# Performance work log

Hardware: AMD Instinct MI355X
Metric: run time of the kernel (lower is better)

## Reference

```python
import jax, jax.numpy as jnp
import numpy as np
from jax import lax

B, C, H, W = 2, 256, 64, 64
KC, RD = C // 8, C // 16  # key_channels=32, GatherExcite rd_channels=16
EPS = 1e-5


def setup_inputs() -> dict:
    key = jax.random.key(0)
    ks = jax.random.split(key, 17)
    s = 0.05
    n = lambda k, shp: jax.random.normal(k, shp, jnp.float32) * s
    return {
        "x": jax.random.normal(ks[0], (B, C, H, W), jnp.float32),
        "Wq": n(ks[1], (KC, C)),
        "Wk": n(ks[2], (KC, C)),
        "Wv": n(ks[3], (C, C)),
        "Wb1": n(ks[4], (KC, C)),
        "Wb2": n(ks[5], (KC, C)),
        "w_gb": jax.random.normal(ks[6], (), jnp.float32),  # 1x1 conv on 1-channel bias map
        "ge_w1": n(ks[7], (RD, C)),
        "ge_b1": jnp.zeros((RD,), jnp.float32),
        "ge_w2": n(ks[8], (C, RD)),
        "ge_b2": jnp.zeros((C,), jnp.float32),
        "Wo": n(ks[9], (C, C)),
        "bn_scale": jnp.ones((C,), jnp.float32),
        "bn_bias": jnp.zeros((C,), jnp.float32),
        "bn_mean": jax.random.normal(ks[10], (C,), jnp.float32) * 0.01,
        "bn_var": jnp.ones((C,), jnp.float32),
        "gamma": jax.random.normal(ks[11], (), jnp.float32) * 0.1,
    }


def _conv1x1(t, w):  # t: [B,Cin,H,W], w: [Cout,Cin]
    return jnp.einsum('bchw,oc->bohw', t, w)


def reference(x, Wq, Wk, Wv, Wb1, Wb2, w_gb, ge_w1, ge_b1, ge_w2, ge_b2,
              Wo, bn_scale, bn_bias, bn_mean, bn_var, gamma):
    b, c, h, w = x.shape
    hw = h * w

    # GatherExcite (extent=0, use_mlp=True, gate=sigmoid): global mean -> ConvMlp -> sigmoid gate
    m = x.mean(axis=(2, 3), keepdims=True)                     # [B,C,1,1]
    g = jax.nn.relu(_conv1x1(m, ge_w1) + ge_b1[None, :, None, None])
    g = _conv1x1(g, ge_w2) + ge_b2[None, :, None, None]
    key_in = x * jax.nn.sigmoid(g)                             # [B,C,H,W]

    value = _conv1x1(x, Wv).reshape(b, c, hw).transpose(0, 2, 1)   # [B,HW,C]
    query = _conv1x1(x, Wq).reshape(b, KC, hw).transpose(0, 2, 1)  # [B,HW,Kc]
    key_f = _conv1x1(key_in, Wk).reshape(b, KC, hw)                # [B,Kc,HW]

    sim = jnp.einsum('bnk,bkm->bnm', query, key_f)                 # [B,HW,HW]

    # bias branch (dropout is identity at eval)
    b1 = jax.nn.relu(_conv1x1(x, Wb1)).reshape(b, KC, hw)          # [B,Kc,HW]
    b2 = jax.nn.relu(_conv1x1(x, Wb2)).reshape(b, KC, hw)          # [B,Kc,HW]
    bias = jnp.einsum('bkn,bkm->bnm', b1, b2)                      # [B,HW,HW]

    # AvgPool2d(k=3, s=1, pad=1, count_include_pad=True) on [B,1,HW,HW]
    pooled = lax.reduce_window(bias[:, None], 0.0, lax.add,
                               (1, 1, 3, 3), (1, 1, 1, 1),
                               [(0, 0), (0, 0), (1, 1), (1, 1)]) / 9.0
    bias_map = jax.nn.sigmoid(w_gb * pooled)[:, 0]                 # [B,HW,HW]

    attn = jax.nn.softmax(sim * bias_map, axis=-1)                 # [B,HW,HW]
    ctx = jnp.einsum('bnm,bmc->bnc', attn, value)                  # [B,HW,C]
    ctx = ctx.transpose(0, 2, 1).reshape(b, c, h, w)

    # W: conv1x1 -> BatchNorm (inference) -> ReLU
    y = _conv1x1(ctx, Wo)
    y = (y - bn_mean[None, :, None, None]) * (bn_scale / jnp.sqrt(bn_var + EPS))[None, :, None, None] \
        + bn_bias[None, :, None, None]
    y = jax.nn.relu(y)

    return gamma * y + x
```

## Files before the change

kernel.cpp:

```cpp
#include <hip/hip_runtime.h>
#include <hip/hip_bf16.h>

typedef __bf16 bf16;
typedef __bf16 v8bf __attribute__((ext_vector_type(8)));
typedef __bf16 v4bf __attribute__((ext_vector_type(4)));
typedef float v4f __attribute__((ext_vector_type(4)));

#define HW 4096
#define CH 256
#define KC 32
#define RD 16
#define NB 2
#define BNEPS 1e-5f
#define VSTRIDE 4224
#define LOG2E 1.4426950408889634f

__device__ __forceinline__ float fexp2(float x) {
#if __has_builtin(__builtin_amdgcn_exp2f)
  return __builtin_amdgcn_exp2f(x);
#else
  return exp2f(x);
#endif
}
__device__ __forceinline__ float frcp(float x) {
#if __has_builtin(__builtin_amdgcn_rcpf)
  return __builtin_amdgcn_rcpf(x);
#else
  return 1.f / x;
#endif
}

#define OFF_MEAN   0u
#define OFF_WKB    4096u
#define OFF_QT     69632u
#define OFF_KT     593920u
#define OFF_BS1    1118208u
#define OFF_BS2    1642496u
#define OFF_VT     2166784u
#define OFF_B1R    6492160u
#define OFF_B2R    7016448u
#define OFF_CTX    7540736u
#define OFF_PACC   11735040u
#define OFF_PL     45289472u
#define OFF_WOBF   45551616u
#define OFF_XBT    45682688u
#define OFF_WALL   49876992u

__global__ __launch_bounds__(256) void k_mean(const float* __restrict__ x,
                                              float* __restrict__ mean) {
  int bc = blockIdx.x;
  const float* px = x + (size_t)bc * HW;
  float s = 0.f;
  for (int i = threadIdx.x; i < HW; i += 256) s += px[i];
  __shared__ float red[256];
  red[threadIdx.x] = s; __syncthreads();
  for (int st = 128; st > 0; st >>= 1) {
    if (threadIdx.x < st) red[threadIdx.x] += red[threadIdx.x + st];
    __syncthreads();
  }
  if (threadIdx.x == 0) mean[bc] = red[0] * (1.0f / HW);
}

__global__ __launch_bounds__(256) void k_gate(const float* __restrict__ mean,
    const float* __restrict__ gw1, const float* __restrict__ gb1,
    const float* __restrict__ gw2, const float* __restrict__ gb2,
    const float* __restrict__ Wk, float* __restrict__ wkb,
    const float* __restrict__ Wo, bf16* __restrict__ wo_bf) {
  if (blockIdx.x >= 2) {
    int i = (blockIdx.x - 2) * 256 + threadIdx.x;
    wo_bf[i] = (bf16)Wo[i];
    return;
  }
  int b = blockIdx.x;
  int t = threadIdx.x;
  __shared__ float ms[CH];
  __shared__ float hid[RD];
  ms[t] = mean[b * CH + t];
  __syncthreads();
  if (t < RD) {
    float a = gb1[t];
    for (int c = 0; c < CH; ++c) a += gw1[t * CH + c] * ms[c];
    hid[t] = fmaxf(a, 0.f);
  }
  __syncthreads();
  float a = gb2[t];
  #pragma unroll
  for (int r = 0; r < RD; ++r) a += gw2[t * RD + r] * hid[r];
  float s = 1.f / (1.f + __expf(-a));
  for (int kk = 0; kk < KC; ++kk)
    wkb[((size_t)b * KC + kk) * CH + t] = Wk[kk * CH + t] * s;
}

__global__ __launch_bounds__(256) void k_prep(const float* __restrict__ x,
    const float* __restrict__ Wq, const float* __restrict__ wkb,
    const float* __restrict__ Wb1, const float* __restrict__ Wb2,
    const float* __restrict__ Wv,
    bf16* __restrict__ xbt, bf16* __restrict__ wall) {
  __shared__ __align__(16) float ts[64][68];
  const int blk = blockIdx.x;
  const int t = threadIdx.x;
  if (blk < 512) {
    const int b  = blk >> 8;
    const int id = blk & 255;
    const int ct = id >> 6, nt = id & 63;
    const int c0 = ct * 64, n0 = nt * 64;
    const int crow = t >> 2, nch = (t & 3) * 16;
    const float* xp = x + ((size_t)(b * CH + c0 + crow)) * HW + n0 + nch;
    #pragma unroll
    for (int i = 0; i < 4; ++i)
      *(v4f*)&ts[crow][nch + i * 4] = *(const v4f*)(xp + i * 4);
    __syncthreads();
    const int nl = t >> 2, cc0 = (t & 3) * 16;
    bf16* dst = xbt + ((size_t)(b * HW + n0 + nl)) * CH + c0 + cc0;
    v8bf o0, o1;
    #pragma unroll
    for (int j = 0; j < 8; ++j) { o0[j] = (bf16)ts[cc0 + j][nl]; o1[j] = (bf16)ts[cc0 + 8 + j][nl]; }
    *(v8bf*)dst = o0;
    *(v8bf*)(dst + 8) = o1;
  } else {
    const int idx = blk - 512;
    const int b = idx / 384, row = idx % 384;
    float v;
    if (row < 32)       v = Wq[row * CH + t] * LOG2E;
    else if (row < 64)  v = wkb[((size_t)b * KC + row - 32) * CH + t];
    else if (row < 96)  v = Wb1[(row - 64) * CH + t];
    else if (row < 128) v = Wb2[(row - 96) * CH + t];
    else                v = Wv[(row - 128) * CH + t];
    wall[((size_t)b * 384 + row) * CH + t] = (bf16)v;
  }
}

__global__ __launch_bounds__(256, 4) void k_proj(
    const bf16* __restrict__ xbt, const bf16* __restrict__ wall,
    bf16* __restrict__ qt, bf16* __restrict__ kt,
    bf16* __restrict__ b1r, bf16* __restrict__ b2r, bf16* __restrict__ vt) {
  __shared__ __align__(16) bf16 xs[32][264];
  __shared__ __align__(16) bf16 tr[4][16][24];
  const int blk = blockIdx.x;
  const int b  = blk >> 9;
  const int bm = (blk >> 7) & 3;
  const int nt = blk & 127;
  const int n0 = nt * 32;
  const int t = threadIdx.x;
  {
    const int row = t >> 3, c0 = (t & 7) * 32;
    const bf16* src = xbt + ((size_t)(b * HW + n0 + row)) * CH + c0;
    #pragma unroll
    for (int i = 0; i < 4; ++i)
      *(v8bf*)&xs[row][c0 + i * 8] = *(const v8bf*)(src + i * 8);
  }
  __syncthreads();
  const int w = t >> 6, lane = t & 63, cl = lane & 15, kh = lane >> 4;
  const int nsub = (w & 1) * 16;
  const int otrio = (w >> 1) * 3;
  const v4f vzero = {0.f, 0.f, 0.f, 0.f};
  v4f acc[3] = {vzero, vzero, vzero};
  const bf16* wb = wall + ((size_t)b * 384 + bm * 96) * CH;
  for (int kk = 0; kk < 8; ++kk) {
    v8bf bx = *(const v8bf*)&xs[nsub + cl][kk * 32 + kh * 8];
    #pragma unroll
    for (int j = 0; j < 3; ++j) {
      v8bf af = *(const v8bf*)(wb + (size_t)((otrio + j) * 16 + cl) * CH + kk * 32 + kh * 8);
      acc[j] = __builtin_amdgcn_mfma_f32_16x16x32_bf16(af, bx, acc[j], 0, 0, 0);
    }
  }
  const int n = n0 + nsub + cl;
  #pragma unroll
  for (int j = 0; j < 3; ++j) {
    const int o0 = bm * 96 + (otrio + j) * 16;
    if (o0 < 128) {
      const bool rel = (o0 >= 64);
      v4bf pk;
      #pragma unroll
      for (int r = 0; r < 4; ++r) {
        float v = acc[j][r];
        if (rel) v = fmaxf(v, 0.f);
        pk[r] = (bf16)v;
      }
      const int seg = o0 >> 5;
      bf16* base = seg == 0 ? qt : seg == 1 ? kt : seg == 2 ? b1r : b2r;
      *(v4bf*)&base[((size_t)b * HW + n) * KC + (o0 & 31) + kh * 4] = pk;
    } else {
      #pragma unroll
      for (int r = 0; r < 4; ++r) tr[w][kh * 4 + r][cl] = (bf16)acc[j][r];
      asm volatile("s_waitcnt lgkmcnt(0)" ::: "memory");
      __builtin_amdgcn_sched_barrier(0);
      const int row = lane >> 2, nch = (lane & 3) * 4;
      v4bf d = *(const v4bf*)&tr[w][row][nch];
      *(v4bf*)&vt[((size_t)b * CH + (o0 - 128) + row) * VSTRIDE + n0 + nsub + nch] = d;
    }
  }
}

__global__ __launch_bounds__(256) void k_pool(const bf16* __restrict__ b1r,
    const bf16* __restrict__ b2r, const float* __restrict__ wgb,
    bf16* __restrict__ bs1, bf16* __restrict__ bs2) {
  int i = blockIdx.x * 256 + threadIdx.x;
  int n = (i >> 5) & (HW - 1);
  float a = (float)b1r[i], c = (float)b2r[i];
  if (n > 0)      { a += (float)b1r[i - KC]; c += (float)b2r[i - KC]; }
  if (n < HW - 1) { a += (float)b1r[i + KC]; c += (float)b2r[i + KC]; }
  const float ws = -LOG2E * wgb[0] * (1.f / 9.f);
  bs1[i] = (bf16)(a * ws);
  bs2[i] = (bf16)c;
}

__global__ __launch_bounds__(256, 3) void k_attn(
    const bf16* __restrict__ qtg, const bf16* __restrict__ ktg,
    const bf16* __restrict__ bs1g, const bf16* __restrict__ bs2g,
    const bf16* __restrict__ vtg,
    bf16* __restrict__ pacc, float* __restrict__ pl) {
  __shared__ __align__(16) bf16 vbuf[256][64];
  __shared__ __align__(16) bf16 kbuf[64][40];
  __shared__ __align__(16) bf16 bbuf[64][40];
  __shared__ __align__(16) bf16 plds[64][72];
  const int blk = blockIdx.x;
  const int rt  = blk >> 3;
  const int os  = blk & 7;
  const int b   = rt >> 6;
  const int row0 = (rt & 63) * 64;
  const int w    = threadIdx.x >> 6;
  const int lane = threadIdx.x & 63;
  const int cl = lane & 15;
  const int kh = lane >> 4;
  const int kb = os * 512;
  const v4f vzero = {0.f, 0.f, 0.f, 0.f};
  const size_t qoff = ((size_t)(b * HW + row0 + w * 16 + cl)) * KC + kh * 8;
  const v8bf qf  = *(const v8bf*)(qtg + qoff);
  const v8bf b1f = *(const v8bf*)(bs1g + qoff);
  const bf16* kt = ktg + (size_t)b * HW * KC;
  const bf16* b2 = bs2g + (size_t)b * HW * KC;
  const bf16* vt = vtg + (size_t)b * CH * VSTRIDE;
  const int krow = w * 16 + (lane >> 2), kslot = (lane & 3) * 8;
  const int vch   = w * 64 + (lane >> 3);
  const int vslog = lane & 7;
  const int vwr   = (vslog ^ (lane >> 3)) * 8;
  const int x7 = cl & 7;
  const int ro0 = (kh ^ x7) * 8;
  const int ro1 = ((kh + 4) ^ x7) * 8;

  *(v8bf*)&kbuf[krow][kslot] = *(const v8bf*)(kt + (size_t)(kb + krow) * KC + kslot);
  *(v8bf*)&bbuf[krow][kslot] = *(const v8bf*)(b2 + (size_t)(kb + krow) * KC + kslot);
  __syncthreads();

  v4f acc[16];
  #pragma unroll
  for (int f = 0; f < 16; ++f) acc[f] = vzero;
  float psum = 0.f;

  for (int s = 0; s < 8; ++s) {
    const int m0 = kb + s * 64;
    v8bf vr[8];
    #pragma unroll
    for (int i = 0; i < 8; ++i)
      vr[i] = *(const v8bf*)(vt + (size_t)(vch + i * 8) * VSTRIDE + m0 + vslog * 8);
    v8bf kr, br;
    if (s < 7) {
      kr = *(const v8bf*)(kt + (size_t)(m0 + 64 + krow) * KC + kslot);
      br = *(const v8bf*)(b2 + (size_t)(m0 + 64 + krow) * KC + kslot);
    }
    #pragma unroll
    for (int cb = 0; cb < 4; ++cb) {
      v8bf kf  = *(const v8bf*)&kbuf[cb * 16 + cl][kh * 8];
      v8bf b2f = *(const v8bf*)&bbuf[cb * 16 + cl][kh * 8];
      v4f sim = __builtin_amdgcn_mfma_f32_16x16x32_bf16(kf,  qf,  vzero, 0, 0, 0);
      v4f bia = __builtin_amdgcn_mfma_f32_16x16x32_bf16(b2f, b1f, vzero, 0, 0, 0);
      v4bf pk;
      #pragma unroll
      for (int r = 0; r < 4; ++r) {
        float bm = frcp(1.f + fexp2(bia[r]));
        float pv = fexp2(sim[r] * bm);
        psum += pv;
        pk[r] = (bf16)pv;
      }
      *(v4bf*)&plds[w * 16 + cl][cb * 16 + kh * 4] = pk;
    }
    #pragma unroll
    for (int i = 0; i < 8; ++i)
      *(v8bf*)&vbuf[vch + i * 8][vwr] = vr[i];
    __syncthreads();
    v8bf vf[8];
    #pragma unroll
    for (int f = 0; f < 4; ++f) {
      vf[f * 2 + 0] = *(const v8bf*)&vbuf[w * 64 + f * 16 + cl][ro0];
      vf[f * 2 + 1] = *(const v8bf*)&vbuf[w * 64 + f * 16 + cl][ro1];
    }
    #pragma unroll
    for (int rg = 0; rg < 4; ++rg) {
      v8bf pa0 = *(const v8bf*)&plds[rg * 16 + cl][kh * 8];
      v8bf pa1 = *(const v8bf*)&plds[rg * 16 + cl][32 + kh * 8];
      #pragma unroll
      for (int f = 0; f < 4; ++f) {
        acc[rg * 4 + f] = __builtin_amdgcn_mfma_f32_16x16x32_bf16(pa0, vf[f * 2 + 0], acc[rg * 4 + f], 0, 0, 0);
        acc[rg * 4 + f] = __builtin_amdgcn_mfma_f32_16x16x32_bf16(pa1, vf[f * 2 + 1], acc[rg * 4 + f], 0, 0, 0);
      }
    }
    if (s < 7) {
      *(v8bf*)&kbuf[krow][kslot] = kr;
      *(v8bf*)&bbuf[krow][kslot] = br;
    }
    __syncthreads();
  }

  {
    float s2 = psum;
    s2 += __shfl_xor(s2, 16);
    s2 += __shfl_xor(s2, 32);
    if (kh == 0) pl[blk * 64 + w * 16 + cl] = s2;
  }
  bf16* po = pacc + (size_t)blk * 64 * CH;
  for (int rg = 0; rg < 4; ++rg) {
    #pragma unroll
    for (int f = 0; f < 4; ++f)
      #pragma unroll
      for (int r = 0; r < 4; ++r)
        plds[w * 16 + kh * 4 + r][f * 16 + cl] = (bf16)acc[rg * 4 + f][r];
    asm volatile("s_waitcnt lgkmcnt(0)" ::: "memory");
    __builtin_amdgcn_sched_barrier(0);
    #pragma unroll
    for (int it = 0; it < 2; ++it) {
      int row = lane >> 2, chunk = it * 4 + (lane & 3);
      v8bf d = *(const v8bf*)&plds[w * 16 + row][chunk * 8];
      *(v8bf*)&po[(size_t)(rg * 16 + row) * CH + w * 64 + chunk * 8] = d;
    }
  }
}

__global__ __launch_bounds__(256) void k_combine(const bf16* __restrict__ pacc,
    const float* __restrict__ pl, bf16* __restrict__ ctx) {
  const int r = blockIdx.x * 4 + (threadIdx.x >> 6);
  const int lane = threadIdx.x & 63;
  const int rt = r >> 6;
  const int rl = r & 63;
  const int base = rt * 8;
  float den = 0.f;
  #pragma unroll
  for (int s = 0; s < 8; ++s) den += pl[(base + s) * 64 + rl];
  const float inv = 1.f / den;
  #pragma unroll
  for (int c0 = 0; c0 < CH; c0 += 64) {
    int c = c0 + lane;
    float a = 0.f;
    #pragma unroll
    for (int s = 0; s < 8; ++s)
      a += (float)pacc[((size_t)(base + s) * 64 + rl) * CH + c];
    ctx[(size_t)r * CH + c] = (bf16)(a * inv);
  }
}

__global__ __launch_bounds__(256) void k_out(
    const bf16* __restrict__ ctx, const bf16* __restrict__ wo,
    const float* __restrict__ bns, const float* __restrict__ bnb,
    const float* __restrict__ bnm, const float* __restrict__ bnv,
    const float* __restrict__ gamma, const float* __restrict__ x,
    float* __restrict__ out) {
  const int blk = blockIdx.x;
  const int n0g = blk * 16;
  const int b   = n0g >> 12;
  const int n0  = n0g & (HW - 1);
  const int t = threadIdx.x;
  const int w = t >> 6, lane = t & 63, cl = lane & 15, kh = lane >> 4;
  const v4f vzero = {0.f, 0.f, 0.f, 0.f};
  v8bf a[8];
  #pragma unroll
  for (int kk = 0; kk < 8; ++kk)
    a[kk] = *(const v8bf*)(ctx + (size_t)(n0g + cl) * CH + kk * 32 + kh * 8);
  v4f acc[4] = {vzero, vzero, vzero, vzero};
  #pragma unroll
  for (int kk = 0; kk < 8; ++kk)
    #pragma unroll
    for (int cg = 0; cg < 4; ++cg) {
      v8bf bfr = *(const v8bf*)(wo + (size_t)(w * 64 + cg * 16 + cl) * CH + kk * 32 + kh * 8);
      acc[cg] = __builtin_amdgcn_mfma_f32_16x16x32_bf16(a[kk], bfr, acc[cg], 0, 0, 0);
    }
  const float g = gamma[0];
  #pragma unroll
  for (int cg = 0; cg < 4; ++cg) {
    int o = w * 64 + cg * 16 + cl;
    float isc = bns[o] / sqrtf(bnv[o] + BNEPS);
    float mu = bnm[o], bb = bnb[o];
    size_t oi = ((size_t)b * CH + o) * HW + n0 + kh * 4;
    v4f xv = *(const v4f*)&x[oi];
    v4f ov;
    #pragma unroll
    for (int r = 0; r < 4; ++r) {
      float v = (acc[cg][r] - mu) * isc + bb;
      v = fmaxf(v, 0.f);
      ov[r] = g * v + xv[r];
    }
    *(v4f*)&out[oi] = ov;
  }
}

extern "C" void kernel_launch(void* const* d_in, const int* in_sizes, int n_in,
                              void* d_out, int out_size, void* d_ws, size_t ws_size,
                              hipStream_t stream) {
  const float* x    = (const float*)d_in[0];
  const float* Wq   = (const float*)d_in[1];
  const float* Wk   = (const float*)d_in[2];
  const float* Wv   = (const float*)d_in[3];
  const float* Wb1  = (const float*)d_in[4];
  const float* Wb2  = (const float*)d_in[5];
  const float* wgb  = (const float*)d_in[6];
  const float* gw1  = (const float*)d_in[7];
  const float* gb1  = (const float*)d_in[8];
  const float* gw2  = (const float*)d_in[9];
  const float* gb2  = (const float*)d_in[10];
  const float* Wo   = (const float*)d_in[11];
  const float* bns  = (const float*)d_in[12];
  const float* bnb  = (const float*)d_in[13];
  const float* bnm  = (const float*)d_in[14];
  const float* bnv  = (const float*)d_in[15];
  const float* gam  = (const float*)d_in[16];

  char* ws = (char*)d_ws;
  float* mean = (float*)(ws + OFF_MEAN);
  float* wkb  = (float*)(ws + OFF_WKB);
  bf16* qt    = (bf16*)(ws + OFF_QT);
  bf16* kt    = (bf16*)(ws + OFF_KT);
  bf16* bs1   = (bf16*)(ws + OFF_BS1);
  bf16* bs2   = (bf16*)(ws + OFF_BS2);
  bf16* vt    = (bf16*)(ws + OFF_VT);
  bf16* b1r   = (bf16*)(ws + OFF_B1R);
  bf16* b2r   = (bf16*)(ws + OFF_B2R);
  bf16* ctx   = (bf16*)(ws + OFF_CTX);
  bf16* pacc  = (bf16*)(ws + OFF_PACC);
  float* plv  = (float*)(ws + OFF_PL);
  bf16* wobf  = (bf16*)(ws + OFF_WOBF);
  bf16* xbt   = (bf16*)(ws + OFF_XBT);
  bf16* wall  = (bf16*)(ws + OFF_WALL);
  float* out  = (float*)d_out;

  hipLaunchKernelGGL(k_mean,    dim3(NB * CH),        dim3(256), 0, stream, x, mean);
  hipLaunchKernelGGL(k_gate,    dim3(2 + 256),        dim3(256), 0, stream, mean, gw1, gb1, gw2, gb2, Wk, wkb, Wo, wobf);
  hipLaunchKernelGGL(k_prep,    dim3(512 + 768),      dim3(256), 0, stream, x, Wq, wkb, Wb1, Wb2, Wv, xbt, wall);
  hipLaunchKernelGGL(k_proj,    dim3(1024),           dim3(256), 0, stream, xbt, wall, qt, kt, b1r, b2r, vt);
  hipLaunchKernelGGL(k_pool,    dim3(NB * HW * KC / 256), dim3(256), 0, stream, b1r, b2r, wgb, bs1, bs2);
  hipLaunchKernelGGL(k_attn,    dim3(1024),           dim3(256), 0, stream, qt, kt, bs1, bs2, vt, pacc, plv);
  hipLaunchKernelGGL(k_combine, dim3(NB * HW / 4),    dim3(256), 0, stream, pacc, plv, ctx);
  hipLaunchKernelGGL(k_out,     dim3(512),            dim3(256), 0, stream, ctx, wobf, bns, bnb, bnm, bnv, gam, x, out);
}
```

Baseline: 93.08 us.

## Fuse mean into prep, gate into weight pack, combine into output GEMM, shrink attn tiles

The channel mean is now computed as per-tile partial sums inside the transpose kernel, and the GatherExcite gate runs inside the weight-pack kernel. This removes the separate mean and gate launches. The split-K combine is folded into the output projection kernel, which drops the ctx round-trip and one more launch. The attention kernel switches to 32-key steps with smaller LDS buffers and a new swizzle so that four blocks can be resident per CU, at the cost of twice as many loop iterations and barriers.

```diff
diff --git a/kernel.cpp b/kernel.cpp
--- a/kernel.cpp
+++ b/kernel.cpp
@@ -30,104 +30,95 @@
 #endif
 }
 
-#define OFF_MEAN   0u
-#define OFF_WKB    4096u
-#define OFF_QT     69632u
-#define OFF_KT     593920u
-#define OFF_BS1    1118208u
-#define OFF_BS2    1642496u
-#define OFF_VT     2166784u
-#define OFF_B1R    6492160u
-#define OFF_B2R    7016448u
-#define OFF_CTX    7540736u
-#define OFF_PACC   11735040u
-#define OFF_PL     45289472u
-#define OFF_WOBF   45551616u
-#define OFF_XBT    45682688u
-#define OFF_WALL   49876992u
-
-__global__ __launch_bounds__(256) void k_mean(const float* __restrict__ x,
-                                              float* __restrict__ mean) {
-  int bc = blockIdx.x;
-  const float* px = x + (size_t)bc * HW;
-  float s = 0.f;
-  for (int i = threadIdx.x; i < HW; i += 256) s += px[i];
-  __shared__ float red[256];
-  red[threadIdx.x] = s; __syncthreads();
-  for (int st = 128; st > 0; st >>= 1) {
-    if (threadIdx.x < st) red[threadIdx.x] += red[threadIdx.x + st];
-    __syncthreads();
-  }
-  if (threadIdx.x == 0) mean[bc] = red[0] * (1.0f / HW);
-}
-
-__global__ __launch_bounds__(256) void k_gate(const float* __restrict__ mean,
+#define OFF_QT     0u
+#define OFF_KT     524288u
+#define OFF_BS1    1048576u
+#define OFF_BS2    1572864u
+#define OFF_VT     2097152u
+#define OFF_B1R    6422528u
+#define OFF_B2R    6946816u
+#define OFF_PACC   7471104u
+#define OFF_PL     41025536u
+#define OFF_WOBF   41287680u
+#define OFF_XBT    41418752u
+#define OFF_WALL   45613056u
+#define OFF_MPART  46006272u
+
+__global__ __launch_bounds__(256) void k_prep(const float* __restrict__ x,
+    bf16* __restrict__ xbt, float* __restrict__ mpart) {
+  __shared__ __align__(16) float ts[64][68];
+  const int blk = blockIdx.x;
+  const int b  = blk >> 8;
+  const int id = blk & 255;
+  const int ct = id >> 6, nt = id & 63;
+  const int c0 = ct * 64, n0 = nt * 64;
+  const int t = threadIdx.x;
+  const int crow = t >> 2, nch = (t & 3) * 16;
+  const float* xp = x + ((size_t)(b * CH + c0 + crow)) * HW + n0 + nch;
+  #pragma unroll
+  for (int i = 0; i < 4; ++i)
+    *(v4f*)&ts[crow][nch + i * 4] = *(const v4f*)(xp + i * 4);
+  __syncthreads();
+  {
+    float p = 0.f;
+    #pragma unroll
+    for (int j = 0; j < 16; ++j) p += ts[crow][nch + j];
+    p += __shfl_xor(p, 1);
+    p += __shfl_xor(p, 2);
+    if ((t & 3) == 0) mpart[(size_t)(b * CH + c0 + crow) * 64 + nt] = p;
+  }
+  const int nl = t >> 2, cc0 = (t & 3) * 16;
+  bf16* dst = xbt + ((size_t)(b * HW + n0 + nl)) * CH + c0 + cc0;
+  v8bf o0, o1;
+  #pragma unroll
+  for (int j = 0; j < 8; ++j) { o0[j] = (bf16)ts[cc0 + j][nl]; o1[j] = (bf16)ts[cc0 + 8 + j][nl]; }
+  *(v8bf*)dst = o0;
+  *(v8bf*)(dst + 8) = o1;
+}
+
+__global__ __launch_bounds__(256) void k_pack(
+    const float* __restrict__ mpart,
     const float* __restrict__ gw1, const float* __restrict__ gb1,
     const float* __restrict__ gw2, const float* __restrict__ gb2,
-    const float* __restrict__ Wk, float* __restrict__ wkb,
-    const float* __restrict__ Wo, bf16* __restrict__ wo_bf) {
-  if (blockIdx.x >= 2) {
-    int i = (blockIdx.x - 2) * 256 + threadIdx.x;
+    const float* __restrict__ Wq, const float* __restrict__ Wk,
+    const float* __restrict__ Wb1, const float* __restrict__ Wb2,
+    const float* __restrict__ Wv, const float* __restrict__ Wo,
+    bf16* __restrict__ wall, bf16* __restrict__ wo_bf) {
+  __shared__ float ms[CH];
+  __shared__ float hid[RD];
+  const int blk = blockIdx.x;
+  const int t = threadIdx.x;
+  if (blk >= 768) {
+    int i = (blk - 768) * 256 + t;
     wo_bf[i] = (bf16)Wo[i];
     return;
   }
-  int b = blockIdx.x;
-  int t = threadIdx.x;
-  __shared__ float ms[CH];
-  __shared__ float hid[RD];
-  ms[t] = mean[b * CH + t];
-  __syncthreads();
-  if (t < RD) {
-    float a = gb1[t];
-    for (int c = 0; c < CH; ++c) a += gw1[t * CH + c] * ms[c];
-    hid[t] = fmaxf(a, 0.f);
-  }
-  __syncthreads();
-  float a = gb2[t];
-  #pragma unroll
-  for (int r = 0; r < RD; ++r) a += gw2[t * RD + r] * hid[r];
-  float s = 1.f / (1.f + __expf(-a));
-  for (int kk = 0; kk < KC; ++kk)
-    wkb[((size_t)b * KC + kk) * CH + t] = Wk[kk * CH + t] * s;
-}
-
-__global__ __launch_bounds__(256) void k_prep(const float* __restrict__ x,
-    const float* __restrict__ Wq, const float* __restrict__ wkb,
-    const float* __restrict__ Wb1, const float* __restrict__ Wb2,
-    const float* __restrict__ Wv,
-    bf16* __restrict__ xbt, bf16* __restrict__ wall) {
-  __shared__ __align__(16) float ts[64][68];
-  const int blk = blockIdx.x;
-  const int t = threadIdx.x;
-  if (blk < 512) {
-    const int b  = blk >> 8;
-    const int id = blk & 255;
-    const int ct = id >> 6, nt = id & 63;
-    const int c0 = ct * 64, n0 = nt * 64;
-    const int crow = t >> 2, nch = (t & 3) * 16;
-    const float* xp = x + ((size_t)(b * CH + c0 + crow)) * HW + n0 + nch;
-    #pragma unroll
-    for (int i = 0; i < 4; ++i)
-      *(v4f*)&ts[crow][nch + i * 4] = *(const v4f*)(xp + i * 4);
+  const int b = blk / 384, row = blk % 384;
+  float v;
+  if (row < 32)       v = Wq[row * CH + t] * LOG2E;
+  else if (row < 64) {
+    float m = 0.f;
+    const float* mp = mpart + (size_t)(b * CH + t) * 64;
+    #pragma unroll
+    for (int j = 0; j < 64; ++j) m += mp[j];
+    ms[t] = m * (1.0f / HW);
     __syncthreads();
-    const int nl = t >> 2, cc0 = (t & 3) * 16;
-    bf16* dst = xbt + ((size_t)(b * HW + n0 + nl)) * CH + c0 + cc0;
-    v8bf o0, o1;
-    #pragma unroll
-    for (int j = 0; j < 8; ++j) { o0[j] = (bf16)ts[cc0 + j][nl]; o1[j] = (bf16)ts[cc0 + 8 + j][nl]; }
-    *(v8bf*)dst = o0;
-    *(v8bf*)(dst + 8) = o1;
-  } else {
-    const int idx = blk - 512;
-    const int b = idx / 384, row = idx % 384;
-    float v;
-    if (row < 32)       v = Wq[row * CH + t] * LOG2E;
-    else if (row < 64)  v = wkb[((size_t)b * KC + row - 32) * CH + t];
-    else if (row < 96)  v = Wb1[(row - 64) * CH + t];
-    else if (row < 128) v = Wb2[(row - 96) * CH + t];
-    else                v = Wv[(row - 128) * CH + t];
-    wall[((size_t)b * 384 + row) * CH + t] = (bf16)v;
-  }
+    if (t < RD) {
+      float a = gb1[t];
+      for (int c = 0; c < CH; ++c) a += gw1[t * CH + c] * ms[c];
+      hid[t] = fmaxf(a, 0.f);
+    }
+    __syncthreads();
+    float a = gb2[t];
+    #pragma unroll
+    for (int r = 0; r < RD; ++r) a += gw2[t * RD + r] * hid[r];
+    float s = 1.f / (1.f + __expf(-a));
+    v = Wk[(row - 32) * CH + t] * s;
+  }
+  else if (row < 96)  v = Wb1[(row - 64) * CH + t];
+  else if (row < 128) v = Wb2[(row - 96) * CH + t];
+  else                v = Wv[(row - 128) * CH + t];
+  wall[((size_t)b * 384 + row) * CH + t] = (bf16)v;
 }
 
 __global__ __launch_bounds__(256, 4) void k_proj(
@@ -205,24 +196,24 @@
   bs2[i] = (bf16)c;
 }
 
-__global__ __launch_bounds__(256, 3) void k_attn(
+__global__ __launch_bounds__(256, 4) void k_attn(
     const bf16* __restrict__ qtg, const bf16* __restrict__ ktg,
     const bf16* __restrict__ bs1g, const bf16* __restrict__ bs2g,
     const bf16* __restrict__ vtg,
     bf16* __restrict__ pacc, float* __restrict__ pl) {
-  __shared__ __align__(16) bf16 vbuf[256][64];
-  __shared__ __align__(16) bf16 kbuf[64][40];
-  __shared__ __align__(16) bf16 bbuf[64][40];
-  __shared__ __align__(16) bf16 plds[64][72];
+  __shared__ __align__(16) bf16 vbuf[128][64];
+  __shared__ __align__(16) bf16 kbuf[32][40];
+  __shared__ __align__(16) bf16 bbuf[32][40];
+  __shared__ __align__(16) bf16 plds[64][40];
   const int blk = blockIdx.x;
   const int rt  = blk >> 3;
   const int os  = blk & 7;
   const int b   = rt >> 6;
   const int row0 = (rt & 63) * 64;
-  const int w    = threadIdx.x >> 6;
-  const int lane = threadIdx.x & 63;
-  const int cl = lane & 15;
-  const int kh = lane >> 4;
+  const int t = threadIdx.x;
+  const int w = t >> 6;
+  const int lane = t & 63;
+  const int cl = lane & 15, kh = lane >> 4;
   const int kb = os * 512;
   const v4f vzero = {0.f, 0.f, 0.f, 0.f};
   const size_t qoff = ((size_t)(b * HW + row0 + w * 16 + cl)) * KC + kh * 8;
@@ -231,16 +222,15 @@
   const bf16* kt = ktg + (size_t)b * HW * KC;
   const bf16* b2 = bs2g + (size_t)b * HW * KC;
   const bf16* vt = vtg + (size_t)b * CH * VSTRIDE;
-  const int krow = w * 16 + (lane >> 2), kslot = (lane & 3) * 8;
-  const int vch   = w * 64 + (lane >> 3);
-  const int vslog = lane & 7;
-  const int vwr   = (vslog ^ (lane >> 3)) * 8;
-  const int x7 = cl & 7;
-  const int ro0 = (kh ^ x7) * 8;
-  const int ro1 = ((kh + 4) ^ x7) * 8;
-
-  *(v8bf*)&kbuf[krow][kslot] = *(const v8bf*)(kt + (size_t)(kb + krow) * KC + kslot);
-  *(v8bf*)&bbuf[krow][kslot] = *(const v8bf*)(b2 + (size_t)(kb + krow) * KC + kslot);
+  const int sr = (t >> 2) & 31, sl = (t & 3) * 8;
+  const bf16* sbase = (t < 128) ? kt : b2;
+  bf16* sdst = (t < 128) ? &kbuf[sr][sl] : &bbuf[sr][sl];
+  const int vsl = lane & 3;
+  const int vslot3 = ((((lane >> 2) & 1) * 4 + vsl) ^ (lane >> 3)) * 8;
+  const int rline = w * 32 + (cl >> 1);
+  const int rslot = ((((cl & 1) * 4) + kh) ^ (cl >> 1)) * 8;
+
+  *(v8bf*)sdst = *(const v8bf*)(sbase + (size_t)(kb + sr) * KC + sl);
   __syncthreads();
 
   v4f acc[16];
@@ -248,19 +238,17 @@
   for (int f = 0; f < 16; ++f) acc[f] = vzero;
   float psum = 0.f;
 
-  for (int s = 0; s < 8; ++s) {
-    const int m0 = kb + s * 64;
-    v8bf vr[8];
-    #pragma unroll
-    for (int i = 0; i < 8; ++i)
-      vr[i] = *(const v8bf*)(vt + (size_t)(vch + i * 8) * VSTRIDE + m0 + vslog * 8);
-    v8bf kr, br;
-    if (s < 7) {
-      kr = *(const v8bf*)(kt + (size_t)(m0 + 64 + krow) * KC + kslot);
-      br = *(const v8bf*)(b2 + (size_t)(m0 + 64 + krow) * KC + kslot);
-    }
-    #pragma unroll
-    for (int cb = 0; cb < 4; ++cb) {
+  for (int s = 0; s < 16; ++s) {
+    const int m0 = kb + s * 32;
+    v8bf vr[4];
+    #pragma unroll
+    for (int i = 0; i < 4; ++i)
+      vr[i] = *(const v8bf*)(vt + (size_t)(w * 64 + i * 16 + (lane >> 2)) * VSTRIDE + m0 + vsl * 8);
+    v8bf pr;
+    if (s < 15)
+      pr = *(const v8bf*)(sbase + (size_t)(m0 + 32 + sr) * KC + sl);
+    #pragma unroll
+    for (int cb = 0; cb < 2; ++cb) {
       v8bf kf  = *(const v8bf*)&kbuf[cb * 16 + cl][kh * 8];
       v8bf b2f = *(const v8bf*)&bbuf[cb * 16 + cl][kh * 8];
       v4f sim = __builtin_amdgcn_mfma_f32_16x16x32_bf16(kf,  qf,  vzero, 0, 0, 0);
@@ -276,29 +264,22 @@
       *(v4bf*)&plds[w * 16 + cl][cb * 16 + kh * 4] = pk;
     }
     #pragma unroll
-    for (int i = 0; i < 8; ++i)
-      *(v8bf*)&vbuf[vch + i * 8][vwr] = vr[i];
+    for (int i = 0; i < 4; ++i)
+      *(v8bf*)&vbuf[w * 32 + i * 8 + (lane >> 3)][vslot3] = vr[i];
     __syncthreads();
-    v8bf vf[8];
-    #pragma unroll
-    for (int f = 0; f < 4; ++f) {
-      vf[f * 2 + 0] = *(const v8bf*)&vbuf[w * 64 + f * 16 + cl][ro0];
-      vf[f * 2 + 1] = *(const v8bf*)&vbuf[w * 64 + f * 16 + cl][ro1];
-    }
-    #pragma unroll
-    for (int rg = 0; rg < 4; ++rg) {
-      v8bf pa0 = *(const v8bf*)&plds[rg * 16 + cl][kh * 8];
-      v8bf pa1 = *(const v8bf*)&plds[rg * 16 + cl][32 + kh * 8];
-      #pragma unroll
-      for (int f = 0; f < 4; ++f) {
-        acc[rg * 4 + f] = __builtin_amdgcn_mfma_f32_16x16x32_bf16(pa0, vf[f * 2 + 0], acc[rg * 4 + f], 0, 0, 0);
-        acc[rg * 4 + f] = __builtin_amdgcn_mfma_f32_16x16x32_bf16(pa1, vf[f * 2 + 1], acc[rg * 4 + f], 0, 0, 0);
-      }
-    }
-    if (s < 7) {
-      *(v8bf*)&kbuf[krow][kslot] = kr;
-      *(v8bf*)&bbuf[krow][kslot] = br;
-    }
+    v8bf vf[4], pa[4];
+    #pragma unroll
+    for (int f = 0; f < 4; ++f)
+      vf[f] = *(const v8bf*)&vbuf[rline + f * 8][rslot];
+    #pragma unroll
+    for (int rg = 0; rg < 4; ++rg)
+      pa[rg] = *(const v8bf*)&plds[rg * 16 + cl][kh * 8];
+    #pragma unroll
+    for (int rg = 0; rg < 4; ++rg)
+      #pragma unroll
+      for (int f = 0; f < 4; ++f)
+        acc[rg * 4 + f] = __builtin_amdgcn_mfma_f32_16x16x32_bf16(pa[rg], vf[f], acc[rg * 4 + f], 0, 0, 0);
+    if (s < 15) *(v8bf*)sdst = pr;
     __syncthreads();
   }
 
@@ -308,48 +289,28 @@
     s2 += __shfl_xor(s2, 32);
     if (kh == 0) pl[blk * 64 + w * 16 + cl] = s2;
   }
+  bf16 (*ep)[64] = (bf16 (*)[64])vbuf;
   bf16* po = pacc + (size_t)blk * 64 * CH;
   for (int rg = 0; rg < 4; ++rg) {
     #pragma unroll
     for (int f = 0; f < 4; ++f)
       #pragma unroll
       for (int r = 0; r < 4; ++r)
-        plds[w * 16 + kh * 4 + r][f * 16 + cl] = (bf16)acc[rg * 4 + f][r];
+        ep[w * 16 + kh * 4 + r][f * 16 + cl] = (bf16)acc[rg * 4 + f][r];
     asm volatile("s_waitcnt lgkmcnt(0)" ::: "memory");
     __builtin_amdgcn_sched_barrier(0);
     #pragma unroll
     for (int it = 0; it < 2; ++it) {
       int row = lane >> 2, chunk = it * 4 + (lane & 3);
-      v8bf d = *(const v8bf*)&plds[w * 16 + row][chunk * 8];
+      v8bf d = *(const v8bf*)&ep[w * 16 + row][chunk * 8];
       *(v8bf*)&po[(size_t)(rg * 16 + row) * CH + w * 64 + chunk * 8] = d;
     }
   }
 }
 
-__global__ __launch_bounds__(256) void k_combine(const bf16* __restrict__ pacc,
-    const float* __restrict__ pl, bf16* __restrict__ ctx) {
-  const int r = blockIdx.x * 4 + (threadIdx.x >> 6);
-  const int lane = threadIdx.x & 63;
-  const int rt = r >> 6;
-  const int rl = r & 63;
-  const int base = rt * 8;
-  float den = 0.f;
-  #pragma unroll
-  for (int s = 0; s < 8; ++s) den += pl[(base + s) * 64 + rl];
-  const float inv = 1.f / den;
-  #pragma unroll
-  for (int c0 = 0; c0 < CH; c0 += 64) {
-    int c = c0 + lane;
-    float a = 0.f;
-    #pragma unroll
-    for (int s = 0; s < 8; ++s)
-      a += (float)pacc[((size_t)(base + s) * 64 + rl) * CH + c];
-    ctx[(size_t)r * CH + c] = (bf16)(a * inv);
-  }
-}
-
-__global__ __launch_bounds__(256) void k_out(
-    const bf16* __restrict__ ctx, const bf16* __restrict__ wo,
+__global__ __launch_bounds__(256) void k_outc(
+    const bf16* __restrict__ pacc, const float* __restrict__ pl,
+    const bf16* __restrict__ wo,
     const float* __restrict__ bns, const float* __restrict__ bnb,
     const float* __restrict__ bnm, const float* __restrict__ bnv,
     const float* __restrict__ gamma, const float* __restrict__ x,
@@ -360,11 +321,26 @@
   const int n0  = n0g & (HW - 1);
   const int t = threadIdx.x;
   const int w = t >> 6, lane = t & 63, cl = lane & 15, kh = lane >> 4;
+  const int base = (blk >> 2) * 8;
+  const int rl = (blk & 3) * 16 + cl;
   const v4f vzero = {0.f, 0.f, 0.f, 0.f};
+  float den = 0.f;
+  #pragma unroll
+  for (int s = 0; s < 8; ++s) den += pl[(base + s) * 64 + rl];
+  const float inv = 1.f / den;
   v8bf a[8];
   #pragma unroll
-  for (int kk = 0; kk < 8; ++kk)
-    a[kk] = *(const v8bf*)(ctx + (size_t)(n0g + cl) * CH + kk * 32 + kh * 8);
+  for (int kk = 0; kk < 8; ++kk) {
+    float sum[8] = {0.f, 0.f, 0.f, 0.f, 0.f, 0.f, 0.f, 0.f};
+    #pragma unroll
+    for (int s = 0; s < 8; ++s) {
+      v8bf pv = *(const v8bf*)&pacc[((size_t)(base + s) * 64 + rl) * CH + kk * 32 + kh * 8];
+      #pragma unroll
+      for (int j = 0; j < 8; ++j) sum[j] += (float)pv[j];
+    }
+    #pragma unroll
+    for (int j = 0; j < 8; ++j) a[kk][j] = (bf16)(sum[j] * inv);
+  }
   v4f acc[4] = {vzero, vzero, vzero, vzero};
   #pragma unroll
   for (int kk = 0; kk < 8; ++kk)
@@ -414,8 +390,6 @@
   const float* gam  = (const float*)d_in[16];
 
   char* ws = (char*)d_ws;
-  float* mean = (float*)(ws + OFF_MEAN);
-  float* wkb  = (float*)(ws + OFF_WKB);
   bf16* qt    = (bf16*)(ws + OFF_QT);
   bf16* kt    = (bf16*)(ws + OFF_KT);
   bf16* bs1   = (bf16*)(ws + OFF_BS1);
@@ -423,20 +397,19 @@
   bf16* vt    = (bf16*)(ws + OFF_VT);
   bf16* b1r   = (bf16*)(ws + OFF_B1R);
   bf16* b2r   = (bf16*)(ws + OFF_B2R);
-  bf16* ctx   = (bf16*)(ws + OFF_CTX);
   bf16* pacc  = (bf16*)(ws + OFF_PACC);
   float* plv  = (float*)(ws + OFF_PL);
   bf16* wobf  = (bf16*)(ws + OFF_WOBF);
   bf16* xbt   = (bf16*)(ws + OFF_XBT);
   bf16* wall  = (bf16*)(ws + OFF_WALL);
+  float* mprt = (float*)(ws + OFF_MPART);
   float* out  = (float*)d_out;
 
-  hipLaunchKernelGGL(k_mean,    dim3(NB * CH),        dim3(256), 0, stream, x, mean);
-  hipLaunchKernelGGL(k_gate,    dim3(2 + 256),        dim3(256), 0, stream, mean, gw1, gb1, gw2, gb2, Wk, wkb, Wo, wobf);
-  hipLaunchKernelGGL(k_prep,    dim3(512 + 768),      dim3(256), 0, stream, x, Wq, wkb, Wb1, Wb2, Wv, xbt, wall);
-  hipLaunchKernelGGL(k_proj,    dim3(1024),           dim3(256), 0, stream, xbt, wall, qt, kt, b1r, b2r, vt);
-  hipLaunchKernelGGL(k_pool,    dim3(NB * HW * KC / 256), dim3(256), 0, stream, b1r, b2r, wgb, bs1, bs2);
-  hipLaunchKernelGGL(k_attn,    dim3(1024),           dim3(256), 0, stream, qt, kt, bs1, bs2, vt, pacc, plv);
-  hipLaunchKernelGGL(k_combine, dim3(NB * HW / 4),    dim3(256), 0, stream, pacc, plv, ctx);
-  hipLaunchKernelGGL(k_out,     dim3(512),            dim3(256), 0, stream, ctx, wobf, bns, bnb, bnm, bnv, gam, x, out);
-}
+  hipLaunchKernelGGL(k_prep, dim3(512),  dim3(256), 0, stream, x, xbt, mprt);
+  hipLaunchKernelGGL(k_pack, dim3(1024), dim3(256), 0, stream, mprt, gw1, gb1, gw2, gb2,
+                     Wq, Wk, Wb1, Wb2, Wv, Wo, wall, wobf);
+  hipLaunchKernelGGL(k_proj, dim3(1024), dim3(256), 0, stream, xbt, wall, qt, kt, b1r, b2r, vt);
+  hipLaunchKernelGGL(k_pool, dim3(NB * HW * KC / 256), dim3(256), 0, stream, b1r, b2r, wgb, bs1, bs2);
+  hipLaunchKernelGGL(k_attn, dim3(1024), dim3(256), 0, stream, qt, kt, bs1, bs2, vt, pacc, plv);
+  hipLaunchKernelGGL(k_outc, dim3(512),  dim3(256), 0, stream, pacc, plv, wobf, bns, bnb, bnm, bnv, gam, x, out);
+}
```

New measurement: 95.65 us. +2.8%, slower.
